# Performance work log

Measured on AMD Instinct MI355X. Metric: run time of the kernel, lower is better.

The kernel has to match this reference:

```python
import jax, jax.numpy as jnp
import numpy as np

B, H, S, D = 4, 16, 2048, 128

def setup_inputs() -> dict:
    key = jax.random.key(0)
    kq, kk, kv = jax.random.split(key, 3)
    q = jax.random.normal(kq, (B, H, S, D), dtype=jnp.float32)
    k = jax.random.normal(kk, (B, H, S, D), dtype=jnp.float32)
    v = jax.random.normal(kv, (B, H, S, D), dtype=jnp.float32)
    # causal mask: True = masked (upper triangle above the diagonal)
    mask = jnp.triu(jnp.ones((S, S), dtype=jnp.bool_), k=1)[None, None, :, :]
    return {"q": q, "k": k, "v": v, "mask": mask}

def reference(q, k, v, mask):
    head_dim = q.shape[-1]
    scale = 1.0 / jnp.sqrt(jnp.float32(head_dim))
    # scores: [B, H, Sq, Sk]
    scores = jnp.einsum('bhqd,bhkd->bhqk', q, k) * scale
    scores = jnp.where(mask, -jnp.inf, scores)
    attention_weights = jax.nn.softmax(scores, axis=-1)
    # dropout p=0.0 (eval): identity
    context_vectors = jnp.einsum('bhqk,bhkd->bhqd', attention_weights, v)
    return (context_vectors, attention_weights)
```

## Files before the change

kernel.cpp:

```cpp
#include <hip/hip_runtime.h>
#include <hip/hip_bf16.h>

#define S_LEN 2048
#define D_DIM 128
#define BH_N  64
#define BR    64
#define BC    64
#define NTILE (S_LEN / BC)
#define SCALE 0.08838834764831845f

typedef __attribute__((ext_vector_type(8)))  short short8;
typedef __attribute__((ext_vector_type(16))) float f32x16;

__device__ __forceinline__ ushort f2bf(float f) {
  union { float f; unsigned u; } x; x.f = f;
  unsigned r = x.u + 0x7FFFu + ((x.u >> 16) & 1u);
  return (ushort)(r >> 16);
}

__device__ __forceinline__ short8 pack8(float4 a, float4 b) {
  short8 p;
  p[0] = (short)f2bf(a.x); p[1] = (short)f2bf(a.y);
  p[2] = (short)f2bf(a.z); p[3] = (short)f2bf(a.w);
  p[4] = (short)f2bf(b.x); p[5] = (short)f2bf(b.y);
  p[6] = (short)f2bf(b.z); p[7] = (short)f2bf(b.w);
  return p;
}

__global__ __launch_bounds__(256, 2) void attn_fused_kernel(
    const float* __restrict__ q, const float* __restrict__ k,
    const float* __restrict__ v, float* __restrict__ ctx,
    float* __restrict__ wts) {
  __shared__ __align__(16) char klds[BC * 256];
  __shared__ __align__(16) char vtlds[D_DIM * 128];
  __shared__ __align__(16) char plds[BR * 128];
  __shared__ float lred[2][BR];

  const int tid  = threadIdx.x;
  const int lane = tid & 63;
  const int w    = tid >> 6;
  const int wq   = w >> 1, wk = w & 1;
  const int l31  = lane & 31, lhi = lane >> 5;

  const int bid = blockIdx.x;
  const int qb  = (NTILE - 1) - (bid >> 6);
  const int bh  = bid & 63;

  const float* qbase = q + (size_t)bh * S_LEN * D_DIM;
  const float* kbase = k + (size_t)bh * S_LEN * D_DIM;
  const float* vbase = v + (size_t)bh * S_LEN * D_DIM;
  float* wtile = wts + (size_t)(bh * S_LEN + qb * BR) * S_LEN;

  short8 qf[8];
  {
    const float* qrow = qbase + (size_t)(qb * BR + wq * 32 + l31) * D_DIM;
    #pragma unroll
    for (int s = 0; s < 8; ++s) {
      int d0 = 16 * s + 8 * lhi;
      float4 a = *(const float4*)(qrow + d0);
      float4 b = *(const float4*)(qrow + d0 + 4);
      qf[s] = pack8(a, b);
    }
  }

  auto stage_k = [&](int kt) {
    int trow = tid >> 2, tc = tid & 3;
    const float* src = kbase + (size_t)(kt * BC + trow) * D_DIM;
    #pragma unroll
    for (int i = 0; i < 4; ++i) {
      int c0 = tc * 8 + i * 32;
      float4 a = *(const float4*)(src + c0);
      float4 b = *(const float4*)(src + c0 + 4);
      int off = (trow * 256 + c0 * 2) ^ ((trow & 7) << 4);
      *(short8*)(klds + off) = pack8(a, b);
    }
  };

  auto stage_v = [&](int kt) {
    int vrow = tid >> 2, tc = tid & 3;
    const float* src = vbase + (size_t)(kt * BC + vrow) * D_DIM;
    #pragma unroll
    for (int i = 0; i < 4; ++i) {
      int c0 = tc * 8 + i * 32;
      float4 a = *(const float4*)(src + c0);
      float4 b = *(const float4*)(src + c0 + 4);
      float fv[8] = {a.x, a.y, a.z, a.w, b.x, b.y, b.z, b.w};
      #pragma unroll
      for (int j = 0; j < 8; ++j) {
        int d = c0 + j;
        int off = (d * 128 + vrow * 2) ^ ((d & 7) << 4);
        *(ushort*)(vtlds + off) = f2bf(fv[j]);
      }
    }
  };

  auto compute_s = [&]() -> f32x16 {
    f32x16 acc;
    #pragma unroll
    for (int i = 0; i < 16; ++i) acc[i] = 0.f;
    int krow = wk * 32 + l31;
    int base = krow * 256;
    int swz  = (krow & 7) << 4;
    #pragma unroll
    for (int s = 0; s < 8; ++s) {
      int off = (base + 32 * s + 16 * lhi) ^ swz;
      short8 kf = *(const short8*)(klds + off);
      acc = __builtin_amdgcn_mfma_f32_32x32x16_bf16(qf[s], kf, acc, 0, 0, 0);
    }
    return acc;
  };

  float l_lane[16];
  #pragma unroll
  for (int r = 0; r < 16; ++r) l_lane[r] = 0.f;

  for (int kt = 0; kt <= qb; ++kt) {
    __syncthreads();
    stage_k(kt);
    __syncthreads();
    f32x16 acc = compute_s();
    int kcol = kt * BC + wk * 32 + l31;
    bool diag = (kt == qb);
    #pragma unroll
    for (int r = 0; r < 16; ++r) {
      int qrow = qb * BR + wq * 32 + (r & 3) + 8 * (r >> 2) + 4 * lhi;
      float val = acc[r] * SCALE;
      l_lane[r] += (diag && kcol > qrow) ? 0.f : __expf(val);
    }
  }

  #pragma unroll
  for (int r = 0; r < 16; ++r) {
    float x = l_lane[r];
    x += __shfl_xor(x, 1);  x += __shfl_xor(x, 2);  x += __shfl_xor(x, 4);
    x += __shfl_xor(x, 8);  x += __shfl_xor(x, 16);
    l_lane[r] = x;
  }
  if (l31 == 0) {
    #pragma unroll
    for (int r = 0; r < 16; ++r) {
      int rl = wq * 32 + (r & 3) + 8 * (r >> 2) + 4 * lhi;
      lred[wk][rl] = l_lane[r];
    }
  }
  __syncthreads();
  float inv_l[16];
  #pragma unroll
  for (int r = 0; r < 16; ++r) {
    int rl = wq * 32 + (r & 3) + 8 * (r >> 2) + 4 * lhi;
    inv_l[r] = 1.0f / (lred[0][rl] + lred[1][rl]);
  }

  f32x16 o0, o1;
  #pragma unroll
  for (int i = 0; i < 16; ++i) { o0[i] = 0.f; o1[i] = 0.f; }

  for (int kt = 0; kt <= qb; ++kt) {
    __syncthreads();
    stage_k(kt);
    stage_v(kt);
    __syncthreads();
    f32x16 acc = compute_s();
    int kcol_l = wk * 32 + l31;
    int kcol = kt * BC + kcol_l;
    bool diag = (kt == qb);
    #pragma unroll
    for (int r = 0; r < 16; ++r) {
      int rl = wq * 32 + (r & 3) + 8 * (r >> 2) + 4 * lhi;
      int qrow = qb * BR + rl;
      float val = acc[r] * SCALE;
      float p = (diag && kcol > qrow) ? 0.f : __expf(val) * inv_l[r];
      wtile[(size_t)rl * S_LEN + kcol] = p;
      int poff = (rl * 128 + kcol_l * 2) ^ ((rl & 7) << 4);
      *(ushort*)(plds + poff) = f2bf(p);
    }
    __syncthreads();
    #pragma unroll
    for (int s = 0; s < 4; ++s) {
      int prow = wq * 32 + l31;
      int paoff = (prow * 128 + (16 * s + 8 * lhi) * 2) ^ ((prow & 7) << 4);
      short8 pa = *(const short8*)(plds + paoff);
      int kko = (16 * s + 8 * lhi) * 2;
      int d0 = wk * 64 + l31;
      int d1 = d0 + 32;
      int off0 = (d0 * 128 + kko) ^ ((d0 & 7) << 4);
      int off1 = (d1 * 128 + kko) ^ ((d1 & 7) << 4);
      short8 vb0 = *(const short8*)(vtlds + off0);
      short8 vb1 = *(const short8*)(vtlds + off1);
      o0 = __builtin_amdgcn_mfma_f32_32x32x16_bf16(pa, vb0, o0, 0, 0, 0);
      o1 = __builtin_amdgcn_mfma_f32_32x32x16_bf16(pa, vb1, o1, 0, 0, 0);
    }
  }

  {
    int zb = (qb + 1) * BC;
    if (zb < S_LEN) {
      int ncol4 = (S_LEN - zb) >> 2;
      float4 z; z.x = z.y = z.z = z.w = 0.f;
      for (int r = 0; r < BR; ++r) {
        float4* bp = (float4*)(wtile + (size_t)r * S_LEN + zb);
        for (int c = tid; c < ncol4; c += 256) bp[c] = z;
      }
    }
  }

  #pragma unroll
  for (int r = 0; r < 16; ++r) {
    int rl = wq * 32 + (r & 3) + 8 * (r >> 2) + 4 * lhi;
    size_t obase = (size_t)(bh * S_LEN + qb * BR + rl) * D_DIM;
    ctx[obase + wk * 64 + l31]      = o0[r];
    ctx[obase + wk * 64 + 32 + l31] = o1[r];
  }
}

extern "C" void kernel_launch(void* const* d_in, const int* in_sizes, int n_in,
                              void* d_out, int out_size, void* d_ws, size_t ws_size,
                              hipStream_t stream) {
  const float* q = (const float*)d_in[0];
  const float* k = (const float*)d_in[1];
  const float* v = (const float*)d_in[2];
  float* ctx = (float*)d_out;
  float* wts = ctx + (size_t)BH_N * S_LEN * D_DIM;
  dim3 grid(BH_N * NTILE);
  attn_fused_kernel<<<grid, dim3(256), 0, stream>>>(q, k, v, ctx, wts);
}
```

Baseline: 673.8 us.

## Split into flash kernel with prefetch plus separate fully-parallel weights kernel

The fused two-pass kernel is replaced by a single-pass flash kernel. It accumulates unnormalized P·V and the row sums, prefetches the next K/V tile into registers, and writes V transposed as packed bf16 pairs. A second kernel launched over query blocks and 128-column chunks recomputes QK^T, normalizes it with the stored row sums, and writes the attention weights, including the zero region. This removes the serial weights write and zero-fill from the causal-imbalanced fused blocks and spreads the large output write across many more blocks. The cost is recomputing QK^T, a second launch, and an extra small workspace buffer.

```diff
diff --git a/kernel.cpp b/kernel.cpp
--- a/kernel.cpp
+++ b/kernel.cpp
@@ -27,10 +27,10 @@
   return p;
 }
 
-__global__ __launch_bounds__(256, 2) void attn_fused_kernel(
+__global__ __launch_bounds__(256, 2) void attn_flash_kernel(
     const float* __restrict__ q, const float* __restrict__ k,
     const float* __restrict__ v, float* __restrict__ ctx,
-    float* __restrict__ wts) {
+    float* __restrict__ lsum_out) {
   __shared__ __align__(16) char klds[BC * 256];
   __shared__ __align__(16) char vtlds[D_DIM * 128];
   __shared__ __align__(16) char plds[BR * 128];
@@ -49,7 +49,6 @@
   const float* qbase = q + (size_t)bh * S_LEN * D_DIM;
   const float* kbase = k + (size_t)bh * S_LEN * D_DIM;
   const float* vbase = v + (size_t)bh * S_LEN * D_DIM;
-  float* wtile = wts + (size_t)(bh * S_LEN + qb * BR) * S_LEN;
 
   short8 qf[8];
   {
@@ -63,34 +62,46 @@
     }
   }
 
-  auto stage_k = [&](int kt) {
+  float4 kreg[8], vreg[8];
+
+  auto load_k = [&](int kt) {
     int trow = tid >> 2, tc = tid & 3;
     const float* src = kbase + (size_t)(kt * BC + trow) * D_DIM;
     #pragma unroll
     for (int i = 0; i < 4; ++i) {
       int c0 = tc * 8 + i * 32;
-      float4 a = *(const float4*)(src + c0);
-      float4 b = *(const float4*)(src + c0 + 4);
-      int off = (trow * 256 + c0 * 2) ^ ((trow & 7) << 4);
-      *(short8*)(klds + off) = pack8(a, b);
-    }
-  };
-
-  auto stage_v = [&](int kt) {
-    int vrow = tid >> 2, tc = tid & 3;
-    const float* src = vbase + (size_t)(kt * BC + vrow) * D_DIM;
+      kreg[2 * i]     = *(const float4*)(src + c0);
+      kreg[2 * i + 1] = *(const float4*)(src + c0 + 4);
+    }
+  };
+  auto write_k = [&]() {
+    int trow = tid >> 2, tc = tid & 3;
     #pragma unroll
     for (int i = 0; i < 4; ++i) {
       int c0 = tc * 8 + i * 32;
-      float4 a = *(const float4*)(src + c0);
-      float4 b = *(const float4*)(src + c0 + 4);
-      float fv[8] = {a.x, a.y, a.z, a.w, b.x, b.y, b.z, b.w};
-      #pragma unroll
-      for (int j = 0; j < 8; ++j) {
-        int d = c0 + j;
-        int off = (d * 128 + vrow * 2) ^ ((d & 7) << 4);
-        *(ushort*)(vtlds + off) = f2bf(fv[j]);
-      }
+      int off = (trow * 256 + c0 * 2) ^ ((trow & 7) << 4);
+      *(short8*)(klds + off) = pack8(kreg[2 * i], kreg[2 * i + 1]);
+    }
+  };
+  auto load_v = [&](int kt) {
+    int kp = tid & 31, dg = tid >> 5;
+    const float* r0 = vbase + (size_t)(kt * BC + 2 * kp) * D_DIM + dg * 16;
+    #pragma unroll
+    for (int i = 0; i < 4; ++i) {
+      vreg[i]     = *(const float4*)(r0 + 4 * i);
+      vreg[4 + i] = *(const float4*)(r0 + D_DIM + 4 * i);
+    }
+  };
+  auto write_v = [&]() {
+    int kp = tid & 31, dg = tid >> 5;
+    #pragma unroll
+    for (int j = 0; j < 16; ++j) {
+      int d = dg * 16 + j;
+      float lo = vreg[j >> 2][j & 3];
+      float hi = vreg[4 + (j >> 2)][j & 3];
+      unsigned u = (unsigned)f2bf(lo) | ((unsigned)f2bf(hi) << 16);
+      int off = (d * 128 + kp * 4) ^ ((d & 7) << 4);
+      *(unsigned*)(vtlds + off) = u;
     }
   };
 
@@ -111,55 +122,17 @@
   };
 
   float l_lane[16];
-  #pragma unroll
-  for (int r = 0; r < 16; ++r) l_lane[r] = 0.f;
+  f32x16 o0, o1;
+  #pragma unroll
+  for (int i = 0; i < 16; ++i) { l_lane[i] = 0.f; o0[i] = 0.f; o1[i] = 0.f; }
+
+  load_k(0); load_v(0);
 
   for (int kt = 0; kt <= qb; ++kt) {
+    write_k(); write_v();
+    if (kt < qb) { load_k(kt + 1); load_v(kt + 1); }
     __syncthreads();
-    stage_k(kt);
-    __syncthreads();
-    f32x16 acc = compute_s();
-    int kcol = kt * BC + wk * 32 + l31;
-    bool diag = (kt == qb);
-    #pragma unroll
-    for (int r = 0; r < 16; ++r) {
-      int qrow = qb * BR + wq * 32 + (r & 3) + 8 * (r >> 2) + 4 * lhi;
-      float val = acc[r] * SCALE;
-      l_lane[r] += (diag && kcol > qrow) ? 0.f : __expf(val);
-    }
-  }
-
-  #pragma unroll
-  for (int r = 0; r < 16; ++r) {
-    float x = l_lane[r];
-    x += __shfl_xor(x, 1);  x += __shfl_xor(x, 2);  x += __shfl_xor(x, 4);
-    x += __shfl_xor(x, 8);  x += __shfl_xor(x, 16);
-    l_lane[r] = x;
-  }
-  if (l31 == 0) {
-    #pragma unroll
-    for (int r = 0; r < 16; ++r) {
-      int rl = wq * 32 + (r & 3) + 8 * (r >> 2) + 4 * lhi;
-      lred[wk][rl] = l_lane[r];
-    }
-  }
-  __syncthreads();
-  float inv_l[16];
-  #pragma unroll
-  for (int r = 0; r < 16; ++r) {
-    int rl = wq * 32 + (r & 3) + 8 * (r >> 2) + 4 * lhi;
-    inv_l[r] = 1.0f / (lred[0][rl] + lred[1][rl]);
-  }
-
-  f32x16 o0, o1;
-  #pragma unroll
-  for (int i = 0; i < 16; ++i) { o0[i] = 0.f; o1[i] = 0.f; }
-
-  for (int kt = 0; kt <= qb; ++kt) {
-    __syncthreads();
-    stage_k(kt);
-    stage_v(kt);
-    __syncthreads();
+
     f32x16 acc = compute_s();
     int kcol_l = wk * 32 + l31;
     int kcol = kt * BC + kcol_l;
@@ -168,13 +141,13 @@
     for (int r = 0; r < 16; ++r) {
       int rl = wq * 32 + (r & 3) + 8 * (r >> 2) + 4 * lhi;
       int qrow = qb * BR + rl;
-      float val = acc[r] * SCALE;
-      float p = (diag && kcol > qrow) ? 0.f : __expf(val) * inv_l[r];
-      wtile[(size_t)rl * S_LEN + kcol] = p;
+      float e = (diag && kcol > qrow) ? 0.f : __expf(acc[r] * SCALE);
+      l_lane[r] += e;
       int poff = (rl * 128 + kcol_l * 2) ^ ((rl & 7) << 4);
-      *(ushort*)(plds + poff) = f2bf(p);
+      *(ushort*)(plds + poff) = f2bf(e);
     }
     __syncthreads();
+
     #pragma unroll
     for (int s = 0; s < 4; ++s) {
       int prow = wq * 32 + l31;
@@ -190,26 +163,109 @@
       o0 = __builtin_amdgcn_mfma_f32_32x32x16_bf16(pa, vb0, o0, 0, 0, 0);
       o1 = __builtin_amdgcn_mfma_f32_32x32x16_bf16(pa, vb1, o1, 0, 0, 0);
     }
-  }
-
-  {
-    int zb = (qb + 1) * BC;
-    if (zb < S_LEN) {
-      int ncol4 = (S_LEN - zb) >> 2;
-      float4 z; z.x = z.y = z.z = z.w = 0.f;
-      for (int r = 0; r < BR; ++r) {
-        float4* bp = (float4*)(wtile + (size_t)r * S_LEN + zb);
-        for (int c = tid; c < ncol4; c += 256) bp[c] = z;
-      }
-    }
-  }
-
+    __syncthreads();
+  }
+
+  #pragma unroll
+  for (int r = 0; r < 16; ++r) {
+    float x = l_lane[r];
+    x += __shfl_xor(x, 1);  x += __shfl_xor(x, 2);  x += __shfl_xor(x, 4);
+    x += __shfl_xor(x, 8);  x += __shfl_xor(x, 16);
+    l_lane[r] = x;
+  }
+  if (l31 == 0) {
+    #pragma unroll
+    for (int r = 0; r < 16; ++r) {
+      int rl = wq * 32 + (r & 3) + 8 * (r >> 2) + 4 * lhi;
+      lred[wk][rl] = l_lane[r];
+    }
+  }
+  __syncthreads();
+
+  if (tid < BR)
+    lsum_out[(size_t)bh * S_LEN + qb * BR + tid] = lred[0][tid] + lred[1][tid];
+
+  float inv_l[16];
+  #pragma unroll
+  for (int r = 0; r < 16; ++r) {
+    int rl = wq * 32 + (r & 3) + 8 * (r >> 2) + 4 * lhi;
+    inv_l[r] = 1.0f / (lred[0][rl] + lred[1][rl]);
+  }
   #pragma unroll
   for (int r = 0; r < 16; ++r) {
     int rl = wq * 32 + (r & 3) + 8 * (r >> 2) + 4 * lhi;
     size_t obase = (size_t)(bh * S_LEN + qb * BR + rl) * D_DIM;
-    ctx[obase + wk * 64 + l31]      = o0[r];
-    ctx[obase + wk * 64 + 32 + l31] = o1[r];
+    ctx[obase + wk * 64 + l31]      = o0[r] * inv_l[r];
+    ctx[obase + wk * 64 + 32 + l31] = o1[r] * inv_l[r];
+  }
+}
+
+__global__ __launch_bounds__(256, 4) void attn_wts_kernel(
+    const float* __restrict__ q, const float* __restrict__ k,
+    const float* __restrict__ lsum, float* __restrict__ wts) {
+  const int bid = blockIdx.x;
+  const int kt2 = bid & 15;
+  const int qb  = (bid >> 4) & 31;
+  const int bh  = bid >> 9;
+
+  float* wtile = wts + ((size_t)(bh * S_LEN + qb * BR)) * S_LEN + kt2 * 128;
+  const int tid = threadIdx.x;
+
+  if (2 * kt2 >= qb + 1) {
+    float4 z; z.x = z.y = z.z = z.w = 0.f;
+    #pragma unroll
+    for (int rr = 0; rr < 64; rr += 8)
+      ((float4*)(wtile + (size_t)(rr + (tid >> 5)) * S_LEN))[tid & 31] = z;
+    return;
+  }
+
+  const int lane = tid & 63;
+  const int w    = tid >> 6;
+  const int wq   = w >> 1, wk = w & 1;
+  const int l31  = lane & 31, lhi = lane >> 5;
+
+  short8 qf[8];
+  {
+    const float* qrow = q + (size_t)(bh * S_LEN + qb * BR + wq * 32 + l31) * D_DIM;
+    #pragma unroll
+    for (int s = 0; s < 8; ++s) {
+      int d0 = 16 * s + 8 * lhi;
+      float4 a = *(const float4*)(qrow + d0);
+      float4 b = *(const float4*)(qrow + d0 + 4);
+      qf[s] = pack8(a, b);
+    }
+  }
+
+  float invl[16];
+  #pragma unroll
+  for (int r = 0; r < 16; ++r) {
+    int rl = wq * 32 + (r & 3) + 8 * (r >> 2) + 4 * lhi;
+    invl[r] = 1.0f / lsum[(size_t)bh * S_LEN + qb * BR + rl];
+  }
+
+  #pragma unroll
+  for (int c = 0; c < 2; ++c) {
+    const int colg_base = kt2 * 128 + wk * 64 + c * 32;
+    const float* krow = k + (size_t)(bh * S_LEN + colg_base + l31) * D_DIM;
+    f32x16 acc;
+    #pragma unroll
+    for (int i = 0; i < 16; ++i) acc[i] = 0.f;
+    #pragma unroll
+    for (int s = 0; s < 8; ++s) {
+      int d0 = 16 * s + 8 * lhi;
+      float4 a = *(const float4*)(krow + d0);
+      float4 b = *(const float4*)(krow + d0 + 4);
+      short8 kf = pack8(a, b);
+      acc = __builtin_amdgcn_mfma_f32_32x32x16_bf16(qf[s], kf, acc, 0, 0, 0);
+    }
+    int colg = colg_base + l31;
+    #pragma unroll
+    for (int r = 0; r < 16; ++r) {
+      int rl = wq * 32 + (r & 3) + 8 * (r >> 2) + 4 * lhi;
+      int rowg = qb * BR + rl;
+      float p = (colg > rowg) ? 0.f : __expf(acc[r] * SCALE) * invl[r];
+      wtile[(size_t)rl * S_LEN + wk * 64 + c * 32 + l31] = p;
+    }
   }
 }
 
@@ -221,6 +277,8 @@
   const float* v = (const float*)d_in[2];
   float* ctx = (float*)d_out;
   float* wts = ctx + (size_t)BH_N * S_LEN * D_DIM;
-  dim3 grid(BH_N * NTILE);
-  attn_fused_kernel<<<grid, dim3(256), 0, stream>>>(q, k, v, ctx, wts);
-}
+  float* lsum = (float*)d_ws;
+
+  attn_flash_kernel<<<dim3(BH_N * NTILE), dim3(256), 0, stream>>>(q, k, v, ctx, lsum);
+  attn_wts_kernel<<<dim3(BH_N * NTILE * (S_LEN / 128)), dim3(256), 0, stream>>>(q, k, lsum, wts);
+}
```

Result: slower. 995.5 us (+47.7%).
